# Kernel tuning notes

Hardware: AMD Instinct MI355X
Metric: run time of the kernel (lower is better)

Reference implementation:

```python
import jax, jax.numpy as jnp
import numpy as np

EMBED, HIDDEN, VOCAB = 512, 512, 32000
B, NPIX, MAXLEN = 64, 196, 32

def setup_inputs() -> dict:
    key = jax.random.key(0)
    ks = jax.random.split(key, 12)
    s = 0.05
    return {
        "encoder_outputs": jax.random.normal(ks[0], (B, NPIX, HIDDEN), jnp.float32),
        "captions": jax.random.randint(ks[1], (B, MAXLEN), 0, VOCAB),
        "embedding": jax.random.normal(ks[2], (VOCAB, EMBED), jnp.float32) * s,
        "W_ih": jax.random.normal(ks[3], (4 * HIDDEN, EMBED), jnp.float32) * s,
        "b_ih": jnp.zeros((4 * HIDDEN,), jnp.float32),
        "W_hh": jax.random.normal(ks[4], (4 * HIDDEN, HIDDEN), jnp.float32) * s,
        "b_hh": jnp.zeros((4 * HIDDEN,), jnp.float32),
        "W_fc": jax.random.normal(ks[5], (VOCAB, HIDDEN), jnp.float32) * s,
        "b_fc": jnp.zeros((VOCAB,), jnp.float32),
        "W_init_h": jax.random.normal(ks[6], (HIDDEN, HIDDEN), jnp.float32) * s,
        "b_init_h": jnp.zeros((HIDDEN,), jnp.float32),
        "W_init_c": jax.random.normal(ks[7], (HIDDEN, HIDDEN), jnp.float32) * s,
        "b_init_c": jnp.zeros((HIDDEN,), jnp.float32),
    }

def reference(encoder_outputs, captions, embedding, W_ih, b_ih, W_hh, b_hh,
              W_fc, b_fc, W_init_h, b_init_h, W_init_c, b_init_c):
    # teacher_forcing_ratio = 0 (val/test path): greedy argmax feeds next token
    batch, max_len = captions.shape
    vocab = W_fc.shape[0]
    summary = encoder_outputs.mean(axis=1)                 # [B, H]
    h = summary @ W_init_h.T + b_init_h                    # [B, H]
    c = summary @ W_init_c.T + b_init_c
    tok0 = captions[:, 0]

    def step(carry, _):
        h, c, tok = carry
        x = embedding[tok]                                 # [B, E]
        gates = x @ W_ih.T + b_ih + h @ W_hh.T + b_hh      # [B, 4H]
        i, f, g, o = jnp.split(gates, 4, axis=-1)          # PyTorch gate order i,f,g,o
        i, f, o = jax.nn.sigmoid(i), jax.nn.sigmoid(f), jax.nn.sigmoid(o)
        g = jnp.tanh(g)
        c2 = f * c + i * g
        h2 = o * jnp.tanh(c2)
        out = h2 @ W_fc.T + b_fc                           # [B, V]
        nxt = jnp.argmax(out, axis=1)
        return (h2, c2, nxt), out

    _, outs = jax.lax.scan(step, (h, c, tok0), None, length=max_len - 1)
    outs = jnp.transpose(outs, (1, 0, 2))                  # [B, max_len-1, V]
    zero0 = jnp.zeros((batch, 1, vocab), outs.dtype)       # outputs[:,0,:] stays zero
    return jnp.concatenate([zero0, outs], axis=1)
```

## Files before the change

kernel.cpp:

```cpp
#include <hip/hip_runtime.h>
#include <stdint.h>

#define EMBED  512
#define HIDDEN 512
#define VOCAB  32000
#define BATCH  64
#define NPIX   196
#define MAXLEN 32
#define NBLK   256
#define NTHR   512
#define NGRP   16

typedef float f32x4 __attribute__((ext_vector_type(4)));
typedef short bf16x8 __attribute__((ext_vector_type(8)));
typedef unsigned short ushort_t;
typedef unsigned long long u64;

__device__ __forceinline__ u64 pack_key(float v, int idx) {
    unsigned u = __float_as_uint(v);
    u = (u & 0x80000000u) ? ~u : (u | 0x80000000u);
    return ((u64)u << 32) | (unsigned)(~(unsigned)idx);
}
__device__ __forceinline__ ushort_t f2bf(float x) {
    unsigned u = __float_as_uint(x);
    unsigned r = (u + 0x7fffu + ((u >> 16) & 1u)) >> 16;
    return (ushort_t)r;
}
__device__ __forceinline__ float bf2f(ushort_t h) {
    return __uint_as_float(((unsigned)h) << 16);
}
__device__ __forceinline__ void cst32(unsigned* p, unsigned v) {
    __hip_atomic_store(p, v, __ATOMIC_RELAXED, __HIP_MEMORY_SCOPE_AGENT);
}
__device__ __forceinline__ u64 cld64(const u64* p) {
    return __hip_atomic_load(p, __ATOMIC_RELAXED, __HIP_MEMORY_SCOPE_AGENT);
}

__device__ __forceinline__ void grid_barrier(unsigned* barws, int k, bool fence) {
    __syncthreads();
    if (threadIdx.x == 0) {
        const int grp = blockIdx.x >> 4;
        const bool leader = (blockIdx.x & 15) == 0;
        unsigned* gc = barws + (k * NGRP + grp) * 16;
        unsigned* rc = barws + 16384 + k * 16;
        unsigned* gf = barws + 17408 + (k * NGRP + grp) * 16;
        if (fence) __threadfence();
        else asm volatile("s_waitcnt vmcnt(0)" ::: "memory");
        if (!leader) {
            __hip_atomic_fetch_add(gc, 1u, __ATOMIC_RELAXED, __HIP_MEMORY_SCOPE_AGENT);
            while (__hip_atomic_fetch_add(gf, 0u, __ATOMIC_RELAXED, __HIP_MEMORY_SCOPE_AGENT) == 0u)
                __builtin_amdgcn_s_sleep(32);
        } else {
            while (__hip_atomic_fetch_add(gc, 0u, __ATOMIC_RELAXED, __HIP_MEMORY_SCOPE_AGENT) < 15u)
                __builtin_amdgcn_s_sleep(8);
            __hip_atomic_fetch_add(rc, 1u, __ATOMIC_RELAXED, __HIP_MEMORY_SCOPE_AGENT);
            while (__hip_atomic_fetch_add(rc, 0u, __ATOMIC_RELAXED, __HIP_MEMORY_SCOPE_AGENT) < (unsigned)NGRP)
                __builtin_amdgcn_s_sleep(8);
            __hip_atomic_fetch_add(gf, 1u, __ATOMIC_RELAXED, __HIP_MEMORY_SCOPE_AGENT);
        }
        asm volatile("" ::: "memory");
    }
    __syncthreads();
}

__global__ void ws_init(unsigned* barws, u64* kslab) {
    const int i = blockIdx.x * 256 + threadIdx.x;
    if (i < 33792) barws[i] = 0u;
    if (i < 31 * 1024) kslab[i] = 0ull;
}

__global__ __launch_bounds__(512, 2) void decode_all(
    const float* __restrict__ enc,
    const int*   __restrict__ captions,
    const float* __restrict__ emb,
    const float* __restrict__ W_ih, const float* __restrict__ b_ih,
    const float* __restrict__ W_hh, const float* __restrict__ b_hh,
    const float* __restrict__ W_fc, const float* __restrict__ b_fc,
    const float* __restrict__ W_init_h, const float* __restrict__ b_init_h,
    const float* __restrict__ W_init_c, const float* __restrict__ b_init_c,
    float* __restrict__ out,
    float* __restrict__ cbuf,
    float* __restrict__ hfs,
    unsigned* __restrict__ hhis,
    unsigned* __restrict__ hlos,
    u64* __restrict__ kslab,
    ushort_t* __restrict__ Whi, ushort_t* __restrict__ Wlo,
    unsigned* __restrict__ barws)
{
    __shared__ float wlds[8 * 1032];
    __shared__ __align__(16) float smem[8448];
    __shared__ u64 kredl[512];

    const int blk = blockIdx.x, tid = threadIdx.x;
    const int lane = tid & 63, w = tid >> 6;
    const int u0 = blk * 2;
    const int r16 = lane & 15, g = lane >> 4;

    for (int i = tid; i < 8192; i += NTHR) {
        const int rowp = i >> 10, off = i & 1023;
        const int uu = rowp >> 2, q = rowp & 3;
        const int j = q * HIDDEN + u0 + uu;
        wlds[rowp * 1032 + off] = (off < 512) ? W_ih[(size_t)j * 512 + off]
                                              : W_hh[(size_t)j * 512 + off - 512];
    }

    {
        const int nfrag = VOCAB * 64;
        for (int i = blk * NTHR + tid; i < nfrag; i += NBLK * NTHR) {
            const int col = i >> 6, kf = i & 63;
            const int kb = kf >> 2, gw = kf & 3;
            const f32x4* src = (const f32x4*)(W_fc + (size_t)col * EMBED + kf * 8);
            f32x4 w0 = src[0], w1 = src[1];
            ushort_t hi[8], lo[8];
#pragma unroll
            for (int e = 0; e < 4; ++e) {
                hi[e] = f2bf(w0[e]);     lo[e] = f2bf(w0[e] - bf2f(hi[e]));
                hi[4+e] = f2bf(w1[e]);   lo[4+e] = f2bf(w1[e] - bf2f(hi[4+e]));
            }
            const size_t d = ((size_t)(((col >> 7) * 8 + ((col >> 4) & 7)) * 16 + kb) * 64
                              + gw * 16 + (col & 15)) * 8;
            *(uint64_t*)&Whi[d]     = *(const uint64_t*)hi;
            *(uint64_t*)&Whi[d + 4] = *(const uint64_t*)(hi + 4);
            *(uint64_t*)&Wlo[d]     = *(const uint64_t*)lo;
            *(uint64_t*)&Wlo[d + 4] = *(const uint64_t*)(lo + 4);
        }
    }

    if (blk < BATCH) {
        const int b = blk;
        {
            float s = 0.f;
            const float* p = enc + (size_t)b * NPIX * HIDDEN + tid;
            for (int px = 0; px < NPIX; ++px) s += p[(size_t)px * HIDDEN];
            smem[tid] = s * (1.0f / NPIX);
        }
        __syncthreads();
        {
            const int j = tid;
            const f32x4* wh = (const f32x4*)(W_init_h + (size_t)j * HIDDEN);
            const f32x4* wc = (const f32x4*)(W_init_c + (size_t)j * HIDDEN);
            float ah = 0.f, ac = 0.f;
            for (int k4 = 0; k4 < HIDDEN / 4; ++k4) {
                f32x4 s4 = *(const f32x4*)&smem[k4 * 4];
                f32x4 a = wh[k4], cc = wc[k4];
                ah += s4[0]*a[0] + s4[1]*a[1] + s4[2]*a[2] + s4[3]*a[3];
                ac += s4[0]*cc[0] + s4[1]*cc[1] + s4[2]*cc[2] + s4[3]*cc[3];
            }
            ah += b_init_h[j];
            hfs[b * HIDDEN + j] = ah;
            cbuf[b * HIDDEN + j] = ac + b_init_c[j];
            ushort_t hh = f2bf(ah), hl = f2bf(ah - bf2f(hh));
            unsigned packed = (unsigned)hh | ((unsigned)hl << 16);
            unsigned pp = __shfl_xor(packed, 1, 64);
            if ((j & 1) == 0) {
                const int u2 = j >> 1;
                const int mt = b >> 4, r16m = b & 15;
                const int kb = u2 >> 4, tl = u2 & 15, gg2 = tl >> 2, jj = tl & 3;
                const size_t d = (size_t)(((kb * 4 + mt) * 64) + gg2 * 16 + r16m) * 4 + jj;
                hhis[d] = (packed & 0xffffu) | ((pp & 0xffffu) << 16);
                hlos[d] = (packed >> 16) | (pp & 0xffff0000u);
            }
        }
        f32x4* o4 = (f32x4*)(out + (size_t)b * MAXLEN * VOCAB);
        f32x4 z = {0.f, 0.f, 0.f, 0.f};
        for (int i = tid; i < VOCAB / 4; i += NTHR) __builtin_nontemporal_store(z, &o4[i]);
    }
    grid_barrier(barws, 0, true);

    for (int t = 0; t < MAXLEN - 1; ++t) {
        const float* hfin  = hfs + (size_t)t * 32768;
        unsigned*    hfout = (unsigned*)(hfs + (size_t)(t + 1) * 32768);
        const unsigned* hhi_t = hhis + (size_t)t * 16384;
        const unsigned* hlo_t = hlos + (size_t)t * 16384;

        {
            const int b = tid >> 3, r = tid & 7, uu = r >> 2, q = r & 3;
            const int rowp = uu * 4 + q;
            const int j = q * HIDDEN + u0 + uu;

            int tok;
            if (t == 0) tok = captions[b * MAXLEN];
            else {
                u64 km = cld64(kslab + (size_t)(t - 1) * 1024 + b * 16);
                tok = (int)(~(unsigned)(km & 0xffffffffull));
            }

            const f32x4* x4 = (const f32x4*)(emb + (size_t)tok * EMBED);
            const f32x4* wih4 = (const f32x4*)(wlds + rowp * 1032);
            const f32x4* whh4 = wih4 + 128;

            float a = 0.f;
            const int hr = tid >> 3, hc = (tid & 7) * 16;
            for (int c = 0; c < 4; ++c) {
                __syncthreads();
                {
                    const f32x4* gp = (const f32x4*)(hfin + (size_t)hr * HIDDEN + c * 128 + hc);
                    f32x4 h0 = gp[0], h1 = gp[1], h2 = gp[2], h3 = gp[3];
                    float* lp = &smem[hr * 132 + hc];
                    *(f32x4*)(lp)      = h0;
                    *(f32x4*)(lp + 4)  = h1;
                    *(f32x4*)(lp + 8)  = h2;
                    *(f32x4*)(lp + 12) = h3;
                }
                __syncthreads();
                const float* hs = smem + b * 132;
#pragma unroll 4
                for (int k4 = 0; k4 < 32; ++k4) {
                    const int kg = c * 32 + k4;
                    f32x4 xv = x4[kg];
                    f32x4 hv = *(const f32x4*)&hs[k4 * 4];
                    f32x4 wA = wih4[kg], vA = whh4[kg];
                    a += xv[0]*wA[0] + xv[1]*wA[1] + xv[2]*wA[2] + xv[3]*wA[3]
                       + hv[0]*vA[0] + hv[1]*vA[1] + hv[2]*vA[2] + hv[3]*vA[3];
                }
            }
            a += b_ih[j] + b_hh[j];

            const int base = (lane & ~7) + uu * 4;
            float gi  = __shfl(a, base + 0, 64);
            float gfv = __shfl(a, base + 1, 64);
            float gg  = __shfl(a, base + 2, 64);
            float go  = __shfl(a, base + 3, 64);
            float i_ = 1.f / (1.f + expf(-gi));
            float f_ = 1.f / (1.f + expf(-gfv));
            float o_ = 1.f / (1.f + expf(-go));
            float g_ = tanhf(gg);
            float cv = cbuf[b * HIDDEN + u0 + uu];
            float c2 = f_ * cv + i_ * g_;
            float h2 = o_ * tanhf(c2);
            if (q == 0) cbuf[b * HIDDEN + u0 + uu] = c2;
            float h2o = __shfl(h2, (lane & ~7) + 4, 64);
            if (r == 0) {
                ushort_t h0h = f2bf(h2),             h1h = f2bf(h2o);
                ushort_t h0l = f2bf(h2 - bf2f(h0h)), h1l = f2bf(h2o - bf2f(h1h));
                const int mt = b >> 4, r16m = b & 15;
                const int kb = blk >> 4, tl = blk & 15, gg2 = tl >> 2, jj = tl & 3;
                const size_t d = (size_t)(((kb * 4 + mt) * 64) + gg2 * 16 + r16m) * 4 + jj;
                cst32((unsigned*)hhis + (size_t)t * 16384 + d,
                      (unsigned)h0h | ((unsigned)h1h << 16));
                cst32((unsigned*)hlos + (size_t)t * 16384 + d,
                      (unsigned)h0l | ((unsigned)h1l << 16));
                cst32(hfout + b * HIDDEN + u0,     __float_as_uint(h2));
                cst32(hfout + b * HIDDEN + u0 + 1, __float_as_uint(h2o));
            }
        }
        grid_barrier(barws, 1 + 2 * t, false);

        if (blk < 250) {
            const int col = blk * 128 + w * 16 + r16;

            f32x4 acc[4];
#pragma unroll
            for (int i = 0; i < 4; ++i) acc[i] = (f32x4){0.f, 0.f, 0.f, 0.f};

            const ushort_t* wb_hi = Whi + ((size_t)(blk * 8 + w) * 16) * 64 * 8 + lane * 8;
            const ushort_t* wb_lo = Wlo + ((size_t)(blk * 8 + w) * 16) * 64 * 8 + lane * 8;

#pragma unroll
            for (int kb = 0; kb < 16; ++kb) {
                bf16x8 Bh = *(const bf16x8*)(wb_hi + (size_t)kb * 512);
                bf16x8 Bl = *(const bf16x8*)(wb_lo + (size_t)kb * 512);
                bf16x8 Ah[4], Al[4];
#pragma unroll
                for (int mt = 0; mt < 4; ++mt) {
                    const size_t d = (size_t)((kb * 4 + mt) * 64 + lane) * 4;
                    Ah[mt] = *(const bf16x8*)(hhi_t + d);
                    Al[mt] = *(const bf16x8*)(hlo_t + d);
                }
#pragma unroll
                for (int mt = 0; mt < 4; ++mt) {
                    acc[mt] = __builtin_amdgcn_mfma_f32_16x16x32_bf16(Al[mt], Bh, acc[mt], 0, 0, 0);
                    acc[mt] = __builtin_amdgcn_mfma_f32_16x16x32_bf16(Ah[mt], Bl, acc[mt], 0, 0, 0);
                    acc[mt] = __builtin_amdgcn_mfma_f32_16x16x32_bf16(Ah[mt], Bh, acc[mt], 0, 0, 0);
                }
            }

            const float bias = b_fc[col];
#pragma unroll
            for (int mt = 0; mt < 4; ++mt) {
                u64 rowkey[4];
#pragma unroll
                for (int reg = 0; reg < 4; ++reg) {
                    const int row = mt * 16 + g * 4 + reg;
                    float v = acc[mt][reg] + bias;
                    __builtin_nontemporal_store(v,
                        &out[(size_t)row * (MAXLEN * VOCAB) + (size_t)(t + 1) * VOCAB + col]);
                    u64 km = pack_key(v, col);
#pragma unroll
                    for (int msk = 8; msk >= 1; msk >>= 1) {
                        u64 o = __shfl_xor(km, msk, 64);
                        km = km > o ? km : o;
                    }
                    rowkey[reg] = km;
                }
                if (r16 == 0) {
#pragma unroll
                    for (int reg = 0; reg < 4; ++reg)
                        kredl[w * 64 + mt * 16 + g * 4 + reg] = rowkey[reg];
                }
            }
            __syncthreads();
            if (w == 0) {
                const int row = lane;
                u64 km = kredl[row];
#pragma unroll
                for (int jj = 1; jj < 8; ++jj) {
                    u64 k = kredl[jj * 64 + row];
                    km = k > km ? k : km;
                }
                __hip_atomic_fetch_max(kslab + (size_t)t * 1024 + row * 16, km,
                                       __ATOMIC_RELAXED, __HIP_MEMORY_SCOPE_AGENT);
            }
        }
        grid_barrier(barws, 2 + 2 * t, false);
    }
}

extern "C" void kernel_launch(void* const* d_in, const int* in_sizes, int n_in,
                              void* d_out, int out_size, void* d_ws, size_t ws_size,
                              hipStream_t stream) {
    const float* enc       = (const float*)d_in[0];
    const int*   captions  = (const int*)  d_in[1];
    const float* emb       = (const float*)d_in[2];
    const float* W_ih      = (const float*)d_in[3];
    const float* b_ih      = (const float*)d_in[4];
    const float* W_hh      = (const float*)d_in[5];
    const float* b_hh      = (const float*)d_in[6];
    const float* W_fc      = (const float*)d_in[7];
    const float* b_fc      = (const float*)d_in[8];
    const float* W_init_h  = (const float*)d_in[9];
    const float* b_init_h  = (const float*)d_in[10];
    const float* W_init_c  = (const float*)d_in[11];
    const float* b_init_c  = (const float*)d_in[12];
    float* out = (float*)d_out;

    char* wsb = (char*)d_ws;
    float*    cbuf  = (float*)(wsb + 0);
    u64*      kslab = (u64*)(wsb + 131072);
    unsigned* barws = (unsigned*)(wsb + 393216);
    float*    hfs   = (float*)(wsb + 1048576);
    unsigned* hhis  = (unsigned*)(wsb + 5242880);
    unsigned* hlos  = (unsigned*)(wsb + 7274496);
    ushort_t* Whi   = (ushort_t*)(wsb + 9437184);
    ushort_t* Wlo   = (ushort_t*)(wsb + 42205184);

    ws_init<<<132, 256, 0, stream>>>(barws, kslab);
    decode_all<<<NBLK, NTHR, 0, stream>>>(
        enc, captions, emb, W_ih, b_ih, W_hh, b_hh, W_fc, b_fc,
        W_init_h, b_init_h, W_init_c, b_init_c,
        out, cbuf, hfs, hhis, hlos, kslab, Whi, Wlo, barws);
}
```

Before: 1.216 ms.

## Compute LSTM gate GEMM with 3-way bf16-split MFMA on 128 blocks

Replaces the scalar FP32 LSTM gate dot products, which read per-block W_ih/W_hh rows from LDS, with MFMA bf16 matrix ops. Inputs and weights are split into three bf16 components and six cross-product MFMAs are summed to keep near-FP32 accuracy. Weights are pre-split into fragment layouts in workspace. The gate phase now runs on 128 blocks, each handling 4 hidden units with a K split across 8 waves and an LDS reduction. The FP32 hidden-state buffer is dropped, and h is stored only as three bf16 planes. This targets the serial per-step LSTM latency, at the cost of extra prologue weight conversion, more global traffic for weights, and fewer active blocks in that phase.

Result: slower. 1.992 ms (+63.8%).

```diff
diff --git a/kernel.cpp b/kernel.cpp
--- a/kernel.cpp
+++ b/kernel.cpp
@@ -34,6 +34,22 @@
 }
 __device__ __forceinline__ u64 cld64(const u64* p) {
     return __hip_atomic_load(p, __ATOMIC_RELAXED, __HIP_MEMORY_SCOPE_AGENT);
+}
+__device__ __forceinline__ void split3_8(f32x4 a, f32x4 b,
+                                         bf16x8& h1, bf16x8& h2, bf16x8& h3) {
+    union { ushort_t s[8]; bf16x8 v; } U1, U2, U3;
+#pragma unroll
+    for (int e = 0; e < 4; ++e) {
+        float v0 = a[e];
+        ushort_t x1 = f2bf(v0); float r1 = v0 - bf2f(x1);
+        ushort_t x2 = f2bf(r1); float r2 = r1 - bf2f(x2);
+        U1.s[e] = x1; U2.s[e] = x2; U3.s[e] = f2bf(r2);
+        float v1 = b[e];
+        ushort_t y1 = f2bf(v1); float s1 = v1 - bf2f(y1);
+        ushort_t y2 = f2bf(s1); float s2 = s1 - bf2f(y2);
+        U1.s[4 + e] = y1; U2.s[4 + e] = y2; U3.s[4 + e] = f2bf(s2);
+    }
+    h1 = U1.v; h2 = U2.v; h3 = U3.v;
 }
 
 __device__ __forceinline__ void grid_barrier(unsigned* barws, int k, bool fence) {
@@ -80,29 +96,21 @@
     const float* __restrict__ W_init_c, const float* __restrict__ b_init_c,
     float* __restrict__ out,
     float* __restrict__ cbuf,
-    float* __restrict__ hfs,
     unsigned* __restrict__ hhis,
     unsigned* __restrict__ hlos,
+    unsigned* __restrict__ hxs,
     u64* __restrict__ kslab,
     ushort_t* __restrict__ Whi, ushort_t* __restrict__ Wlo,
+    ushort_t* __restrict__ WG1, ushort_t* __restrict__ WG2, ushort_t* __restrict__ WG3,
     unsigned* __restrict__ barws)
 {
-    __shared__ float wlds[8 * 1032];
-    __shared__ __align__(16) float smem[8448];
+    __shared__ __align__(16) float smem[7168];
     __shared__ u64 kredl[512];
+    __shared__ int ltoks[BATCH];
 
     const int blk = blockIdx.x, tid = threadIdx.x;
     const int lane = tid & 63, w = tid >> 6;
-    const int u0 = blk * 2;
     const int r16 = lane & 15, g = lane >> 4;
-
-    for (int i = tid; i < 8192; i += NTHR) {
-        const int rowp = i >> 10, off = i & 1023;
-        const int uu = rowp >> 2, q = rowp & 3;
-        const int j = q * HIDDEN + u0 + uu;
-        wlds[rowp * 1032 + off] = (off < 512) ? W_ih[(size_t)j * 512 + off]
-                                              : W_hh[(size_t)j * 512 + off - 512];
-    }
 
     {
         const int nfrag = VOCAB * 64;
@@ -123,6 +131,23 @@
             *(uint64_t*)&Whi[d + 4] = *(const uint64_t*)(hi + 4);
             *(uint64_t*)&Wlo[d]     = *(const uint64_t*)lo;
             *(uint64_t*)&Wlo[d + 4] = *(const uint64_t*)(lo + 4);
+        }
+    }
+    {
+        const int nfragG = 128 * 32 * 64;
+        for (int i = blk * NTHR + tid; i < nfragG; i += NBLK * NTHR) {
+            const int blkg = i >> 11, kq = (i >> 6) & 31, lfrag = i & 63;
+            const int g2 = lfrag >> 4, r16f = lfrag & 15;
+            const int u = blkg * 4 + (r16f >> 2);
+            const int j = (r16f & 3) * 512 + u;
+            const int k0 = kq * 32 + g2 * 8;
+            const float* src = (k0 < 512) ? (W_ih + (size_t)j * EMBED + k0)
+                                          : (W_hh + (size_t)j * HIDDEN + (k0 - 512));
+            bf16x8 b1, b2, b3;
+            split3_8(*(const f32x4*)src, *(const f32x4*)(src + 4), b1, b2, b3);
+            *(bf16x8*)&WG1[(size_t)i * 8] = b1;
+            *(bf16x8*)&WG2[(size_t)i * 8] = b2;
+            *(bf16x8*)&WG3[(size_t)i * 8] = b3;
         }
     }
 
@@ -147,18 +172,22 @@
                 ac += s4[0]*cc[0] + s4[1]*cc[1] + s4[2]*cc[2] + s4[3]*cc[3];
             }
             ah += b_init_h[j];
-            hfs[b * HIDDEN + j] = ah;
             cbuf[b * HIDDEN + j] = ac + b_init_c[j];
-            ushort_t hh = f2bf(ah), hl = f2bf(ah - bf2f(hh));
-            unsigned packed = (unsigned)hh | ((unsigned)hl << 16);
-            unsigned pp = __shfl_xor(packed, 1, 64);
+            ushort_t c1 = f2bf(ah); float r1 = ah - bf2f(c1);
+            ushort_t c2 = f2bf(r1); float r2 = r1 - bf2f(c2);
+            ushort_t c3 = f2bf(r2);
+            unsigned p1 = c1, p2 = c2, p3 = c3;
+            unsigned q1 = __shfl_xor(p1, 1, 64);
+            unsigned q2 = __shfl_xor(p2, 1, 64);
+            unsigned q3 = __shfl_xor(p3, 1, 64);
             if ((j & 1) == 0) {
                 const int u2 = j >> 1;
                 const int mt = b >> 4, r16m = b & 15;
                 const int kb = u2 >> 4, tl = u2 & 15, gg2 = tl >> 2, jj = tl & 3;
                 const size_t d = (size_t)(((kb * 4 + mt) * 64) + gg2 * 16 + r16m) * 4 + jj;
-                hhis[d] = (packed & 0xffffu) | ((pp & 0xffffu) << 16);
-                hlos[d] = (packed >> 16) | (pp & 0xffff0000u);
+                hhis[d] = p1 | (q1 << 16);
+                hlos[d] = p2 | (q2 << 16);
+                hxs [d] = p3 | (q3 << 16);
             }
         }
         f32x4* o4 = (f32x4*)(out + (size_t)b * MAXLEN * VOCAB);
@@ -168,85 +197,135 @@
     grid_barrier(barws, 0, true);
 
     for (int t = 0; t < MAXLEN - 1; ++t) {
-        const float* hfin  = hfs + (size_t)t * 32768;
-        unsigned*    hfout = (unsigned*)(hfs + (size_t)(t + 1) * 32768);
-        const unsigned* hhi_t = hhis + (size_t)t * 16384;
-        const unsigned* hlo_t = hlos + (size_t)t * 16384;
-
-        {
-            const int b = tid >> 3, r = tid & 7, uu = r >> 2, q = r & 3;
-            const int rowp = uu * 4 + q;
-            const int j = q * HIDDEN + u0 + uu;
-
-            int tok;
-            if (t == 0) tok = captions[b * MAXLEN];
-            else {
-                u64 km = cld64(kslab + (size_t)(t - 1) * 1024 + b * 16);
-                tok = (int)(~(unsigned)(km & 0xffffffffull));
-            }
-
-            const f32x4* x4 = (const f32x4*)(emb + (size_t)tok * EMBED);
-            const f32x4* wih4 = (const f32x4*)(wlds + rowp * 1032);
-            const f32x4* whh4 = wih4 + 128;
-
-            float a = 0.f;
-            const int hr = tid >> 3, hc = (tid & 7) * 16;
-            for (int c = 0; c < 4; ++c) {
-                __syncthreads();
-                {
-                    const f32x4* gp = (const f32x4*)(hfin + (size_t)hr * HIDDEN + c * 128 + hc);
-                    f32x4 h0 = gp[0], h1 = gp[1], h2 = gp[2], h3 = gp[3];
-                    float* lp = &smem[hr * 132 + hc];
-                    *(f32x4*)(lp)      = h0;
-                    *(f32x4*)(lp + 4)  = h1;
-                    *(f32x4*)(lp + 8)  = h2;
-                    *(f32x4*)(lp + 12) = h3;
-                }
-                __syncthreads();
-                const float* hs = smem + b * 132;
-#pragma unroll 4
-                for (int k4 = 0; k4 < 32; ++k4) {
-                    const int kg = c * 32 + k4;
-                    f32x4 xv = x4[kg];
-                    f32x4 hv = *(const f32x4*)&hs[k4 * 4];
-                    f32x4 wA = wih4[kg], vA = whh4[kg];
-                    a += xv[0]*wA[0] + xv[1]*wA[1] + xv[2]*wA[2] + xv[3]*wA[3]
-                       + hv[0]*vA[0] + hv[1]*vA[1] + hv[2]*vA[2] + hv[3]*vA[3];
-                }
-            }
-            a += b_ih[j] + b_hh[j];
-
-            const int base = (lane & ~7) + uu * 4;
-            float gi  = __shfl(a, base + 0, 64);
-            float gfv = __shfl(a, base + 1, 64);
-            float gg  = __shfl(a, base + 2, 64);
-            float go  = __shfl(a, base + 3, 64);
-            float i_ = 1.f / (1.f + expf(-gi));
-            float f_ = 1.f / (1.f + expf(-gfv));
-            float o_ = 1.f / (1.f + expf(-go));
-            float g_ = tanhf(gg);
-            float cv = cbuf[b * HIDDEN + u0 + uu];
-            float c2 = f_ * cv + i_ * g_;
-            float h2 = o_ * tanhf(c2);
-            if (q == 0) cbuf[b * HIDDEN + u0 + uu] = c2;
-            float h2o = __shfl(h2, (lane & ~7) + 4, 64);
-            if (r == 0) {
-                ushort_t h0h = f2bf(h2),             h1h = f2bf(h2o);
-                ushort_t h0l = f2bf(h2 - bf2f(h0h)), h1l = f2bf(h2o - bf2f(h1h));
-                const int mt = b >> 4, r16m = b & 15;
-                const int kb = blk >> 4, tl = blk & 15, gg2 = tl >> 2, jj = tl & 3;
-                const size_t d = (size_t)(((kb * 4 + mt) * 64) + gg2 * 16 + r16m) * 4 + jj;
-                cst32((unsigned*)hhis + (size_t)t * 16384 + d,
-                      (unsigned)h0h | ((unsigned)h1h << 16));
-                cst32((unsigned*)hlos + (size_t)t * 16384 + d,
-                      (unsigned)h0l | ((unsigned)h1l << 16));
-                cst32(hfout + b * HIDDEN + u0,     __float_as_uint(h2));
-                cst32(hfout + b * HIDDEN + u0 + 1, __float_as_uint(h2o));
+        const unsigned* gi1 = hhis + (size_t)t * 16384;
+        const unsigned* gi2 = hlos + (size_t)t * 16384;
+        const unsigned* gi3 = hxs  + (size_t)t * 16384;
+        unsigned* go1 = hhis + (size_t)(t + 1) * 16384;
+        unsigned* go2 = hlos + (size_t)(t + 1) * 16384;
+        unsigned* go3 = hxs  + (size_t)(t + 1) * 16384;
+
+        if (blk < 128) {
+            if (tid < BATCH) {
+                int tok;
+                if (t == 0) tok = captions[tid * MAXLEN];
+                else {
+                    u64 km = cld64(kslab + (size_t)(t - 1) * 1024 + tid * 16);
+                    tok = (int)(~(unsigned)(km & 0xffffffffull));
+                }
+                ltoks[tid] = tok;
+            }
+            __syncthreads();
+
+            f32x4 acc[4];
+#pragma unroll
+            for (int i = 0; i < 4; ++i) acc[i] = (f32x4){0.f, 0.f, 0.f, 0.f};
+
+            const int ks = w;
+            int tok4[4];
+            if (ks < 4) {
+#pragma unroll
+                for (int mt = 0; mt < 4; ++mt) tok4[mt] = ltoks[mt * 16 + r16];
+            }
+#pragma unroll
+            for (int kk = 0; kk < 4; ++kk) {
+                const int kq = ks * 4 + kk;
+                const size_t bd = ((size_t)(blk * 32 + kq) * 64 + lane) * 8;
+                bf16x8 B1 = *(const bf16x8*)(WG1 + bd);
+                bf16x8 B2 = *(const bf16x8*)(WG2 + bd);
+                bf16x8 B3 = *(const bf16x8*)(WG3 + bd);
+                bf16x8 A1[4], A2[4], A3[4];
+                if (ks < 4) {
+#pragma unroll
+                    for (int mt = 0; mt < 4; ++mt) {
+                        const float* xp = emb + (size_t)tok4[mt] * EMBED + kq * 32 + g * 8;
+                        split3_8(*(const f32x4*)xp, *(const f32x4*)(xp + 4),
+                                 A1[mt], A2[mt], A3[mt]);
+                    }
+                } else {
+                    const int khh = kq - 16;
+#pragma unroll
+                    for (int mt = 0; mt < 4; ++mt) {
+                        const size_t d = (size_t)((khh * 4 + mt) * 64 + lane) * 4;
+                        A1[mt] = *(const bf16x8*)(gi1 + d);
+                        A2[mt] = *(const bf16x8*)(gi2 + d);
+                        A3[mt] = *(const bf16x8*)(gi3 + d);
+                    }
+                }
+#pragma unroll
+                for (int mt = 0; mt < 4; ++mt) {
+                    acc[mt] = __builtin_amdgcn_mfma_f32_16x16x32_bf16(A3[mt], B1, acc[mt], 0, 0, 0);
+                    acc[mt] = __builtin_amdgcn_mfma_f32_16x16x32_bf16(A1[mt], B3, acc[mt], 0, 0, 0);
+                    acc[mt] = __builtin_amdgcn_mfma_f32_16x16x32_bf16(A2[mt], B2, acc[mt], 0, 0, 0);
+                    acc[mt] = __builtin_amdgcn_mfma_f32_16x16x32_bf16(A2[mt], B1, acc[mt], 0, 0, 0);
+                    acc[mt] = __builtin_amdgcn_mfma_f32_16x16x32_bf16(A1[mt], B2, acc[mt], 0, 0, 0);
+                    acc[mt] = __builtin_amdgcn_mfma_f32_16x16x32_bf16(A1[mt], B1, acc[mt], 0, 0, 0);
+                }
+            }
+            if (w != 0) {
+                float* slab = smem + (w - 1) * 1024;
+#pragma unroll
+                for (int mt = 0; mt < 4; ++mt)
+#pragma unroll
+                    for (int reg = 0; reg < 4; ++reg)
+                        slab[(mt * 4 + reg) * 64 + lane] = acc[mt][reg];
+            }
+            __syncthreads();
+            if (w == 0) {
+#pragma unroll
+                for (int mt = 0; mt < 4; ++mt)
+#pragma unroll
+                    for (int reg = 0; reg < 4; ++reg) {
+                        float s = acc[mt][reg];
+#pragma unroll
+                        for (int jw = 0; jw < 7; ++jw)
+                            s += smem[jw * 1024 + (mt * 4 + reg) * 64 + lane];
+                        acc[mt][reg] = s;
+                    }
+                const int u_loc = r16 >> 2, q = r16 & 3;
+                const int U = blk * 4 + u_loc;
+                const float biasl = b_ih[q * 512 + U] + b_hh[q * 512 + U];
+#pragma unroll
+                for (int mt = 0; mt < 4; ++mt)
+#pragma unroll
+                    for (int reg = 0; reg < 4; ++reg) {
+                        float v = acc[mt][reg] + biasl;
+                        const int base = lane & ~3;
+                        float gvi = __shfl(v, base + 0, 64);
+                        float gvf = __shfl(v, base + 1, 64);
+                        float gvg = __shfl(v, base + 2, 64);
+                        float gvo = __shfl(v, base + 3, 64);
+                        const int b = mt * 16 + g * 4 + reg;
+                        float cv = (q == 0) ? cbuf[b * HIDDEN + U] : 0.f;
+                        float i_ = 1.f / (1.f + expf(-gvi));
+                        float f_ = 1.f / (1.f + expf(-gvf));
+                        float g_ = tanhf(gvg);
+                        float o_ = 1.f / (1.f + expf(-gvo));
+                        float c2 = f_ * cv + i_ * g_;
+                        float h2 = o_ * tanhf(c2);
+                        if (q == 0) cbuf[b * HIDDEN + U] = c2;
+                        ushort_t c1s = f2bf(h2); float r1 = h2 - bf2f(c1s);
+                        ushort_t c2s = f2bf(r1); float r2 = r1 - bf2f(c2s);
+                        ushort_t c3s = f2bf(r2);
+                        unsigned w1 = c1s, w2 = c2s, w3 = c3s;
+                        unsigned p1 = __shfl_xor(w1, 4, 64);
+                        unsigned p2 = __shfl_xor(w2, 4, 64);
+                        unsigned p3 = __shfl_xor(w3, 4, 64);
+                        if (q == 0 && (u_loc & 1) == 0) {
+                            const int u2 = blk * 2 + (u_loc >> 1);
+                            const int kb = u2 >> 4, tl = u2 & 15, gg2 = tl >> 2, jj = tl & 3;
+                            const size_t d = (size_t)((kb * 4 + mt) * 64 + gg2 * 16 + (b & 15)) * 4 + jj;
+                            cst32(go1 + d, w1 | (p1 << 16));
+                            cst32(go2 + d, w2 | (p2 << 16));
+                            cst32(go3 + d, w3 | (p3 << 16));
+                        }
+                    }
             }
         }
         grid_barrier(barws, 1 + 2 * t, false);
 
         if (blk < 250) {
+            const unsigned* fhi = hhis + (size_t)(t + 1) * 16384;
+            const unsigned* flo = hlos + (size_t)(t + 1) * 16384;
             const int col = blk * 128 + w * 16 + r16;
 
             f32x4 acc[4];
@@ -264,8 +343,8 @@
 #pragma unroll
                 for (int mt = 0; mt < 4; ++mt) {
                     const size_t d = (size_t)((kb * 4 + mt) * 64 + lane) * 4;
-                    Ah[mt] = *(const bf16x8*)(hhi_t + d);
-                    Al[mt] = *(const bf16x8*)(hlo_t + d);
+                    Ah[mt] = *(const bf16x8*)(fhi + d);
+                    Al[mt] = *(const bf16x8*)(flo + d);
                 }
 #pragma unroll
                 for (int mt = 0; mt < 4; ++mt) {
@@ -338,15 +417,18 @@
     float*    cbuf  = (float*)(wsb + 0);
     u64*      kslab = (u64*)(wsb + 131072);
     unsigned* barws = (unsigned*)(wsb + 393216);
-    float*    hfs   = (float*)(wsb + 1048576);
-    unsigned* hhis  = (unsigned*)(wsb + 5242880);
-    unsigned* hlos  = (unsigned*)(wsb + 7274496);
-    ushort_t* Whi   = (ushort_t*)(wsb + 9437184);
-    ushort_t* Wlo   = (ushort_t*)(wsb + 42205184);
+    unsigned* hhis  = (unsigned*)(wsb + 1048576);
+    unsigned* hlos  = (unsigned*)(wsb + 3145728);
+    unsigned* hxs   = (unsigned*)(wsb + 5242880);
+    ushort_t* WG1   = (ushort_t*)(wsb + 7340032);
+    ushort_t* WG2   = (ushort_t*)(wsb + 11534336);
+    ushort_t* WG3   = (ushort_t*)(wsb + 15728640);
+    ushort_t* Whi   = (ushort_t*)(wsb + 19922944);
+    ushort_t* Wlo   = (ushort_t*)(wsb + 52690944);
 
     ws_init<<<132, 256, 0, stream>>>(barws, kslab);
     decode_all<<<NBLK, NTHR, 0, stream>>>(
         enc, captions, emb, W_ih, b_ih, W_hh, b_hh, W_fc, b_fc,
         W_init_h, b_init_h, W_init_c, b_init_c,
-        out, cbuf, hfs, hhis, hlos, kslab, Whi, Wlo, barws);
-}
+        out, cbuf, hhis, hlos, hxs, kslab, Whi, Wlo, WG1, WG2, WG3, barws);
+}
```
